# Performance work log

Measured on AMD Instinct MI355X. Metric: run time of the kernel, lower is better.

The kernel has to match this reference:

```python
import jax, jax.numpy as jnp
import numpy as np

# Complete binary Huffman tree: V leaves, V-1 internal nodes, heap-indexed
# (node 0 = root, leaf i lives at heap index V-1+i, parent(n) = (n-1)//2).
V = 32768     # vocab size (leaves)
D = 15        # path depth = log2(V) internal nodes per leaf
DM = 1024     # input word-vector dim
B = 8         # batch of input word vectors
T = 1024      # target ids per batch item


def _build_paths():
    """paths[i, l] = heap index of the l-th internal node (leaf-to-root) on leaf i's path."""
    n = np.arange(V, dtype=np.int64) + (V - 1)  # leaf heap indices
    paths = np.zeros((V, D), dtype=np.int32)
    for lvl in range(D):
        n = (n - 1) // 2
        paths[:, lvl] = n
    return jnp.asarray(paths)


def setup_inputs() -> dict:
    key = jax.random.key(0)
    k1, k2, k3 = jax.random.split(key, 3)
    x = jax.random.normal(k1, (B, DM), dtype=jnp.float32)
    ids = jax.random.randint(k2, (B, T), 0, V)
    W = jax.random.normal(k3, (V - 1, DM), dtype=jnp.float32) * 0.02  # stacked Linear(DM,1) weights
    b = jnp.zeros((V - 1,), dtype=jnp.float32)                        # stacked Linear biases
    return {"x": x, "ids": ids, "paths": _build_paths(), "W": W, "b": b}


def reference(x, ids, paths, W, b):
    # node_idx: [B, T, D] internal-node heap indices along each target's path
    node_idx = paths[ids]
    Wp = W[node_idx]                 # [B, T, D, DM] gathered per-node weight rows
    bp = b[node_idx]                 # [B, T, D]
    # per-node Linear + bias: logit = w_node . x + b_node
    logits = jnp.einsum('btdk,bk->btd', Wp, x) + bp
    # product of sigmoid branch probabilities along the path -> [B, T]
    return jnp.prod(jax.nn.sigmoid(logits), axis=-1)
```

## Files before the change

### kernel.cpp

```cpp
#include <hip/hip_runtime.h>
#include <math.h>

#define V 32768
#define D 15
#define DM 1024
#define B 8
#define T 1024
#define NNODES (V - 1)
#define R 4

typedef float vfloat4 __attribute__((ext_vector_type(4)));

__global__ __launch_bounds__(256, 4) void hsm_logits_kernel(
    const float* __restrict__ x,
    const float* __restrict__ W,
    const float* __restrict__ bias,
    float* __restrict__ sig)
{
    __shared__ vfloat4 xs[B * DM / 4];

    const vfloat4* x4 = (const vfloat4*)x;
    #pragma unroll
    for (int i = threadIdx.x; i < B * DM / 4; i += 256) xs[i] = x4[i];
    __syncthreads();

    const int wave = __builtin_amdgcn_readfirstlane(threadIdx.x >> 6);
    const int lane = threadIdx.x & 63;
    const int rowbase = blockIdx.x * 32 + wave * 8;

    const vfloat4* Wb = (const vfloat4*)W;

    vfloat4 wv[R], wvn[R];
    float acc[R * B];

    #pragma unroll
    for (int r = 0; r < R; r++) {
        int row = rowbase + r;
        if (row > NNODES - 1) row = NNODES - 1;
        wv[r] = __builtin_nontemporal_load(&Wb[(size_t)row * 256 + lane]);
    }

    auto run_pass = [&](int prow0, bool preload_next, int nrow0) {
        #pragma unroll
        for (int i = 0; i < R * B; i++) acc[i] = 0.f;
        #pragma unroll
        for (int j = 0; j < 4; j++) {
            if (j < 3) {
                #pragma unroll
                for (int r = 0; r < R; r++) {
                    int row = prow0 + r;
                    if (row > NNODES - 1) row = NNODES - 1;
                    wvn[r] = __builtin_nontemporal_load(
                        &Wb[(size_t)row * 256 + (j + 1) * 64 + lane]);
                }
            } else if (preload_next) {
                #pragma unroll
                for (int r = 0; r < R; r++) {
                    int row = nrow0 + r;
                    if (row > NNODES - 1) row = NNODES - 1;
                    wvn[r] = __builtin_nontemporal_load(
                        &Wb[(size_t)row * 256 + lane]);
                }
            }
            vfloat4 xv[B];
            #pragma unroll
            for (int b = 0; b < B; b++) xv[b] = xs[b * 256 + j * 64 + lane];
            #pragma unroll
            for (int r = 0; r < R; r++) {
                #pragma unroll
                for (int b = 0; b < B; b++) {
                    acc[r * 8 + b] += wv[r].x * xv[b].x + wv[r].y * xv[b].y +
                                      wv[r].z * xv[b].z + wv[r].w * xv[b].w;
                }
            }
            #pragma unroll
            for (int r = 0; r < R; r++) wv[r] = wvn[r];
        }
    };

#define FOLD_LEVEL(MASK, NOUT)                                   \
    _Pragma("unroll")                                            \
    for (int i = 0; i < (NOUT); i++) {                           \
        const float lo = acc[2 * i];                             \
        const float hi = acc[2 * i + 1];                         \
        const float send = (lane & (MASK)) ? lo : hi;            \
        const float keep = (lane & (MASK)) ? hi : lo;            \
        acc[i] = keep + __shfl_xor(send, (MASK), 64);            \
    }

    auto fold_store = [&](int prow0) {
        FOLD_LEVEL(1, 16)
        FOLD_LEVEL(2, 8)
        FOLD_LEVEL(4, 4)
        FOLD_LEVEL(8, 2)
        FOLD_LEVEL(16, 1)
        acc[0] += __shfl_xor(acc[0], 32, 64);
        if (lane < 32) {
            const int r = lane >> 3;
            const int b = lane & 7;
            const int row = prow0 + r;
            if (row < NNODES) {
                const float z = acc[0] + bias[row];
                sig[(size_t)row * B + b] = 1.f / (1.f + expf(-z));
            }
        }
    };

    run_pass(rowbase, true, rowbase + R);
    fold_store(rowbase);
    run_pass(rowbase + R, false, 0);
    fold_store(rowbase + R);
#undef FOLD_LEVEL
}

__global__ __launch_bounds__(256) void hsm_prod_kernel(
    const int* __restrict__ ids,
    const int* __restrict__ paths,
    const float* __restrict__ sig,
    float* __restrict__ out)
{
    const int i = blockIdx.x * blockDim.x + threadIdx.x;
    if (i >= B * T) return;
    const int b = i / T;
    const int id = ids[i];
    const int* p = paths + (size_t)id * D;
    const int4* p4 = (const int4*)p;
    int4 n0 = p4[0], n1 = p4[1], n2 = p4[2];
    float prod = 1.f;
    prod *= sig[(size_t)n0.x * B + b] * sig[(size_t)n0.y * B + b] *
            sig[(size_t)n0.z * B + b] * sig[(size_t)n0.w * B + b];
    prod *= sig[(size_t)n1.x * B + b] * sig[(size_t)n1.y * B + b] *
            sig[(size_t)n1.z * B + b] * sig[(size_t)n1.w * B + b];
    prod *= sig[(size_t)n2.x * B + b] * sig[(size_t)n2.y * B + b] *
            sig[(size_t)n2.z * B + b] * sig[(size_t)n2.w * B + b];
    prod *= sig[(size_t)p[12] * B + b] * sig[(size_t)p[13] * B + b] *
            sig[(size_t)p[14] * B + b];
    out[i] = prod;
}

extern "C" void kernel_launch(void* const* d_in, const int* in_sizes, int n_in,
                              void* d_out, int out_size, void* d_ws, size_t ws_size,
                              hipStream_t stream) {
    const float* x     = (const float*)d_in[0];
    const int*   ids   = (const int*)d_in[1];
    const int*   paths = (const int*)d_in[2];
    const float* W     = (const float*)d_in[3];
    const float* bias  = (const float*)d_in[4];
    float* out = (float*)d_out;
    float* sig = (float*)d_ws;

    const int grid1 = (V + 31) / 32;
    hsm_logits_kernel<<<grid1, 256, 0, stream>>>(x, W, bias, sig);

    const int grid2 = (B * T + 255) / 256;
    hsm_prod_kernel<<<grid2, 256, 0, stream>>>(ids, paths, sig, out);
}
```

Before: 197.5 us.

## Skip weight rows for internal nodes not on any target path

Adds a bitmap of which internal nodes are referenced. The bitmap starts with the top 1023 nodes (heap levels 0-9) always set, and a new marking kernel sets the deeper nodes found in the first five path entries of each target. The logits kernel reads the bitmap per wave and only loads W rows and stores sigmoids for marked nodes. With 8192 targets, about 40% of the deepest-level nodes go unused, so this cuts HBM traffic on the W stream. It costs two extra launches and atomics, and the per-wave row predication may leave some wavefronts partially idle.

```diff
diff --git a/kernel.cpp b/kernel.cpp
--- a/kernel.cpp
+++ b/kernel.cpp
@@ -11,11 +11,36 @@
 
 typedef float vfloat4 __attribute__((ext_vector_type(4)));
 
+#define BITMAP_OFF (1u << 20)
+
+__global__ __launch_bounds__(256) void hsm_init_bitmap(unsigned* __restrict__ bm) {
+    const int i = blockIdx.x * 256 + threadIdx.x;
+    if (i < 1024) bm[i] = (i < 31) ? 0xFFFFFFFFu : (i == 31 ? 0x7FFFFFFFu : 0u);
+}
+
+__global__ __launch_bounds__(256) void hsm_mark_kernel(
+    const int* __restrict__ ids,
+    const int* __restrict__ paths,
+    unsigned* __restrict__ bm)
+{
+    const int i = blockIdx.x * 256 + threadIdx.x;
+    if (i >= B * T) return;
+    const int* p = paths + (size_t)ids[i] * D;
+    #pragma unroll
+    for (int d = 0; d < 5; d++) {
+        const int node = p[d];
+        const unsigned w = ((unsigned)node) >> 5;
+        const unsigned m = 1u << (node & 31);
+        if (!(bm[w] & m)) atomicOr(&bm[w], m);
+    }
+}
+
 __global__ __launch_bounds__(256, 4) void hsm_logits_kernel(
     const float* __restrict__ x,
     const float* __restrict__ W,
     const float* __restrict__ bias,
-    float* __restrict__ sig)
+    float* __restrict__ sig,
+    const unsigned* __restrict__ bm)
 {
     __shared__ vfloat4 xs[B * DM / 4];
 
@@ -28,6 +53,9 @@
     const int lane = threadIdx.x & 63;
     const int rowbase = blockIdx.x * 32 + wave * 8;
 
+    const unsigned nbits = __builtin_amdgcn_readfirstlane(
+        (bm[((unsigned)rowbase) >> 5] >> (rowbase & 31)) & 0xFFu);
+
     const vfloat4* Wb = (const vfloat4*)W;
 
     vfloat4 wv[R], wvn[R];
@@ -37,10 +65,12 @@
     for (int r = 0; r < R; r++) {
         int row = rowbase + r;
         if (row > NNODES - 1) row = NNODES - 1;
-        wv[r] = __builtin_nontemporal_load(&Wb[(size_t)row * 256 + lane]);
+        if ((nbits >> r) & 1)
+            wv[r] = __builtin_nontemporal_load(&Wb[(size_t)row * 256 + lane]);
     }
 
-    auto run_pass = [&](int prow0, bool preload_next, int nrow0) {
+    auto run_pass = [&](int prow0, unsigned pb, bool preload_next, int nrow0,
+                        unsigned nb) {
         #pragma unroll
         for (int i = 0; i < R * B; i++) acc[i] = 0.f;
         #pragma unroll
@@ -50,16 +80,18 @@
                 for (int r = 0; r < R; r++) {
                     int row = prow0 + r;
                     if (row > NNODES - 1) row = NNODES - 1;
-                    wvn[r] = __builtin_nontemporal_load(
-                        &Wb[(size_t)row * 256 + (j + 1) * 64 + lane]);
+                    if ((pb >> r) & 1)
+                        wvn[r] = __builtin_nontemporal_load(
+                            &Wb[(size_t)row * 256 + (j + 1) * 64 + lane]);
                 }
             } else if (preload_next) {
                 #pragma unroll
                 for (int r = 0; r < R; r++) {
                     int row = nrow0 + r;
                     if (row > NNODES - 1) row = NNODES - 1;
-                    wvn[r] = __builtin_nontemporal_load(
-                        &Wb[(size_t)row * 256 + lane]);
+                    if ((nb >> r) & 1)
+                        wvn[r] = __builtin_nontemporal_load(
+                            &Wb[(size_t)row * 256 + lane]);
                 }
             }
             vfloat4 xv[B];
@@ -88,7 +120,7 @@
         acc[i] = keep + __shfl_xor(send, (MASK), 64);            \
     }
 
-    auto fold_store = [&](int prow0) {
+    auto fold_store = [&](int prow0, unsigned pb) {
         FOLD_LEVEL(1, 16)
         FOLD_LEVEL(2, 8)
         FOLD_LEVEL(4, 4)
@@ -99,17 +131,18 @@
             const int r = lane >> 3;
             const int b = lane & 7;
             const int row = prow0 + r;
-            if (row < NNODES) {
+            if (((pb >> r) & 1) && row < NNODES) {
                 const float z = acc[0] + bias[row];
                 sig[(size_t)row * B + b] = 1.f / (1.f + expf(-z));
             }
         }
     };
 
-    run_pass(rowbase, true, rowbase + R);
-    fold_store(rowbase);
-    run_pass(rowbase + R, false, 0);
-    fold_store(rowbase + R);
+    const unsigned b0 = nbits & 0xF, b1 = (nbits >> 4) & 0xF;
+    run_pass(rowbase, b0, true, rowbase + R, b1);
+    fold_store(rowbase, b0);
+    run_pass(rowbase + R, b1, false, 0, 0);
+    fold_store(rowbase + R, b1);
 #undef FOLD_LEVEL
 }
 
@@ -148,9 +181,13 @@
     const float* bias  = (const float*)d_in[4];
     float* out = (float*)d_out;
     float* sig = (float*)d_ws;
+    unsigned* bm = (unsigned*)((char*)d_ws + BITMAP_OFF);
+
+    hsm_init_bitmap<<<4, 256, 0, stream>>>(bm);
+    hsm_mark_kernel<<<(B * T + 255) / 256, 256, 0, stream>>>(ids, paths, bm);
 
     const int grid1 = (V + 31) / 32;
-    hsm_logits_kernel<<<grid1, 256, 0, stream>>>(x, W, bias, sig);
+    hsm_logits_kernel<<<grid1, 256, 0, stream>>>(x, W, bias, sig, bm);
 
     const int grid2 = (B * T + 255) / 256;
     hsm_prod_kernel<<<grid2, 256, 0, stream>>>(ids, paths, sig, out);
```

Measured after the change: 250.3 us. 26.7% more time.
